# Kernel tuning notes

Measured on AMD Instinct MI355X. Metric: run time of the kernel, lower is better.

Reference implementation:

```python
import jax, jax.numpy as jnp
import numpy as np

N = 100000
E = 1600000
IN_C, HID_C, OUT_C = 64, 64, 32


def setup_inputs() -> dict:
    key = jax.random.key(0)
    ks = jax.random.split(key, 8)
    x = jax.random.normal(ks[0], (N, IN_C), dtype=jnp.float32)
    edge_index = jax.random.randint(ks[1], (2, E), 0, N, dtype=jnp.int64)
    # GCNConv weights (glorot-ish scale) and biases
    W1 = jax.random.normal(ks[2], (IN_C, HID_C), dtype=jnp.float32) / np.sqrt(IN_C)
    b1 = jnp.zeros((HID_C,), dtype=jnp.float32)
    W2 = jax.random.normal(ks[3], (HID_C, HID_C), dtype=jnp.float32) / np.sqrt(HID_C)
    b2 = jnp.zeros((HID_C,), dtype=jnp.float32)
    Wlin = jax.random.normal(ks[4], (HID_C, OUT_C), dtype=jnp.float32) / np.sqrt(HID_C)
    blin = jnp.zeros((OUT_C,), dtype=jnp.float32)
    return {"x": x, "edge_index": edge_index, "W1": W1, "b1": b1,
            "W2": W2, "b2": b2, "Wlin": Wlin, "blin": blin}


def _gcn_norm(edge_index):
    # PyG GCNConv default: add self-loops, symmetric normalization.
    loop = jnp.arange(N, dtype=edge_index.dtype)
    row = jnp.concatenate([edge_index[0], loop])  # source nodes [E+N]
    col = jnp.concatenate([edge_index[1], loop])  # target nodes [E+N]
    deg = jax.ops.segment_sum(jnp.ones_like(col, dtype=jnp.float32), col,
                              num_segments=N)
    dinv = jnp.where(deg > 0, deg ** -0.5, 0.0)
    norm = dinv[row] * dinv[col]  # [E+N]
    return row, col, norm


def _gcn_conv(h, W, b, row, col, norm):
    h = h @ W                                  # [N, F_out]
    msg = h[row] * norm[:, None]               # gather + scale, [E+N, F_out]
    out = jax.ops.segment_sum(msg, col, num_segments=N)  # scatter-add
    return out + b


def reference(x, edge_index, W1, b1, W2, b2, Wlin, blin):
    row, col, norm = _gcn_norm(edge_index)
    h = jax.nn.relu(_gcn_conv(x, W1, b1, row, col, norm))
    h = jax.nn.relu(_gcn_conv(h, W2, b2, row, col, norm))
    return h @ Wlin + blin
```

## Files before the change

kernel.cpp:

```cpp
#include <hip/hip_runtime.h>
#include <hip/hip_fp16.h>

#define IN_C 64
#define HID_C 64
#define OUT_C 32
#define S_NODES  512
#define S_CAP  12288
#define CHUNK_E 4096

typedef _Float16 f16_t;
typedef f16_t f16x2 __attribute__((ext_vector_type(2)));

__device__ __forceinline__ float dot2(unsigned int a, unsigned int b, float c) {
#if __has_builtin(__builtin_amdgcn_fdot2)
    return __builtin_amdgcn_fdot2(*(f16x2*)&a, *(f16x2*)&b, c, false);
#else
    float2 af = __half22float2(*(__half2*)&a);
    float2 bf = __half22float2(*(__half2*)&b);
    return fmaf(af.x, bf.x, fmaf(af.y, bf.y, c));
#endif
}

__device__ __forceinline__ void mix2(float& s0, float& s1, unsigned int p, float w) {
    asm("v_fma_mix_f32 %0, %2, %3, %0 op_sel:[0,0,0] op_sel_hi:[1,0,0]\n\t"
        "v_fma_mix_f32 %1, %2, %3, %1 op_sel:[1,0,0] op_sel_hi:[1,0,0]"
        : "+v"(s0), "+v"(s1)
        : "v"(p), "v"(w));
}

__device__ __forceinline__ int wave_iscan(int x, int lane) {
#pragma unroll
    for (int o = 1; o < 64; o <<= 1) {
        int y = __shfl_up(x, o);
        if (lane >= o) x += y;
    }
    return x;
}

__global__ __launch_bounds__(256) void fat(const void* ei, int E,
                                           int* bcur, int NB,
                                           int* __restrict__ staging,
                                           int NEB, int GB,
                                           const float* __restrict__ x,
                                           const float* __restrict__ W1,
                                           float* __restrict__ t32, int n,
                                           const float* __restrict__ W2,
                                           const float* __restrict__ Wlin,
                                           unsigned short* __restrict__ Wh2,
                                           unsigned short* __restrict__ Whl) {
    __shared__ __align__(16) int smem[5128];
    int tid = threadIdx.x;
    int b = blockIdx.x;
    if (b < NEB) {
        int* cnt = smem;          int* boff = smem + 256;
        int* lcur = smem + 512;   int* gbase = smem + 768;
        int* stg = smem + 1024;
        int* ps64 = smem + 5120;
        int* wsum = smem + 5121;
        int lane = tid & 63, wv = tid >> 6;
        if (tid == 0) *ps64 = 1;
        cnt[tid] = 0;
        __syncthreads();
        if (2 * tid + 1 < 2 * E && ((const int*)ei)[2 * tid + 1] != 0) *ps64 = 0;
        __syncthreads();
        int is64 = *ps64;
        int e0 = b * CHUNK_E;
        int e1 = min(E, e0 + CHUNK_E);
        const int* ei32 = (const int*)ei;
        int rbuf[16];
        int bbuf[16];
        if (is64) {
#pragma unroll
            for (int k = 0; k < 16; k++) {
                int e = e0 + (k << 8) + tid;
                if (e < e1) {
                    int src = ei32[2 * e];
                    int dst = ei32[2 * (E + e)];
                    rbuf[k] = src | ((dst & 511) << 17);
                    int bk = dst >> 9;
                    bbuf[k] = bk;
                    atomicAdd(&cnt[bk], 1);
                } else bbuf[k] = -1;
            }
        } else {
#pragma unroll
            for (int k = 0; k < 16; k++) {
                int e = e0 + (k << 8) + tid;
                if (e < e1) {
                    int src = ei32[e];
                    int dst = ei32[E + e];
                    rbuf[k] = src | ((dst & 511) << 17);
                    int bk = dst >> 9;
                    bbuf[k] = bk;
                    atomicAdd(&cnt[bk], 1);
                } else bbuf[k] = -1;
            }
        }
        __syncthreads();
        int v = cnt[tid];
        int xx = wave_iscan(v, lane);
        if (lane == 63) wsum[wv] = xx;
        __syncthreads();
        int add = 0;
#pragma unroll
        for (int w = 0; w < 3; w++) add += (w < wv) ? wsum[w] : 0;
        int bo = xx + add - v;
        boff[tid] = bo;
        lcur[tid] = bo;
        __syncthreads();
#pragma unroll
        for (int k = 0; k < 16; k++) {
            if (bbuf[k] >= 0) {
                int p = atomicAdd(&lcur[bbuf[k]], 1);
                stg[p] = rbuf[k];
            }
        }
        __syncthreads();
        if (tid < NB && cnt[tid] > 0) gbase[tid] = atomicAdd(&bcur[tid], cnt[tid]);
        __syncthreads();
        int sw = tid >> 4, sl = tid & 15;
        for (int bk = sw; bk < NB; bk += 16) {
            int c = cnt[bk];
            if (c == 0) continue;
            int o = boff[bk], g = gbase[bk];
            size_t gb = (size_t)bk * S_CAP;
            for (int j = sl; j < c; j += 16) {
                if (g + j < S_CAP) staging[gb + g + j] = stg[o + j];
            }
        }
    } else if (b < NEB + GB) {
        uint4* sA = (uint4*)smem;
        int bb = b - NEB;
        int lane = tid & 63, wave = tid >> 6;
        unsigned int wu[32];
#pragma unroll
        for (int k = 0; k < 32; k++) {
            f16x2 p;
            p.x = (f16_t)W1[(2 * k) * 64 + lane];
            p.y = (f16_t)W1[(2 * k + 1) * 64 + lane];
            wu[k] = *(unsigned int*)&p;
        }
        int base = bb * 64;
        const float2* A2 = (const float2*)x;
        int lim = n * 32;
        for (int i = tid; i < 2048; i += 256) {
            int gi = base * 32 + i;
            float2 v = (gi < lim) ? A2[gi] : make_float2(0.f, 0.f);
            ((__half2*)sA)[i] = __floats2half2_rn(v.x, v.y);
        }
        __syncthreads();
        int r0 = base + wave * 16;
        int r1 = min(r0 + 16, n);
        for (int r = r0; r < r1; r++) {
            int rr = r - base;
            float a0 = 0.f, a1 = 0.f;
#pragma unroll
            for (int j = 0; j < 8; j++) {
                uint4 u = sA[rr * 8 + j];
                a0 = dot2(u.x, wu[4 * j], a0);
                a1 = dot2(u.y, wu[4 * j + 1], a1);
                a0 = dot2(u.z, wu[4 * j + 2], a0);
                a1 = dot2(u.w, wu[4 * j + 3], a1);
            }
            t32[(size_t)r * 64 + lane] = a0 + a1;
        }
    } else {
        for (int i = tid; i < 4096; i += 256) {
            int r = i >> 6, c = i & 63;
            f16_t h2 = (f16_t)W2[r * 64 + c];
            Wh2[c * 64 + r] = *(unsigned short*)&h2;
        }
        for (int i = tid; i < 2048; i += 256) {
            int r = i >> 5, c = i & 31;
            f16_t h = (f16_t)Wlin[r * 32 + c];
            Whl[c * 64 + r] = *(unsigned short*)&h;
        }
    }
}

__global__ __launch_bounds__(1024) void place_fine(const int* __restrict__ staging,
                                                   const int* __restrict__ bcur,
                                                   int* __restrict__ offs,
                                                   float* __restrict__ dinv,
                                                   int* __restrict__ rec,
                                                   const float* __restrict__ t32,
                                                   unsigned short* __restrict__ t16,
                                                   int N, int NB) {
    __shared__ int sdeg[S_NODES];
    __shared__ int curs[S_NODES];
    __shared__ int sb[256];
    __shared__ float sdinv[S_NODES];
    __shared__ int wsum[16];
    int tid = threadIdx.x;
    int lane = tid & 63, wv = tid >> 6;
    if (tid < S_NODES) sdeg[tid] = 0;
    if (tid < 256) {
        int v = (tid < NB) ? min(bcur[tid], S_CAP) : 0;
        int xx = wave_iscan(v, lane);
        if (lane == 63) wsum[wv] = xx;
        sb[tid] = xx;
    }
    __syncthreads();
    if (tid < 256) {
        int add = 0;
#pragma unroll
        for (int w = 0; w < 3; w++) add += (w < wv) ? wsum[w] : 0;
        sb[tid] += add;
    }
    __syncthreads();
    int cnt = min(bcur[blockIdx.x], S_CAP);
    int bbase = sb[blockIdx.x] - cnt;
    if (blockIdx.x == NB - 1 && tid == 0) offs[N] = sb[255];
    int base = blockIdx.x * S_NODES;
    int nn = min(S_NODES, N - base);
    size_t sbase = (size_t)blockIdx.x * S_CAP;
    for (int j = tid; j < cnt; j += 1024) atomicAdd(&sdeg[staging[sbase + j] >> 17], 1);
    __syncthreads();
    int d = (tid < S_NODES) ? sdeg[tid] : 0;
    int x2 = wave_iscan(d, lane);
    if (tid < S_NODES && lane == 63) wsum[wv] = x2;
    __syncthreads();
    if (tid < S_NODES) {
        int add2 = 0;
#pragma unroll
        for (int w = 0; w < 7; w++) add2 += (w < wv) ? wsum[w] : 0;
        int pre = bbase + x2 + add2 - d;
        curs[tid] = pre;
        float dv = rsqrtf((float)(d + 1));
        sdinv[tid] = dv;
        if (tid < nn) {
            offs[base + tid] = pre;
            dinv[base + tid] = dv;
        }
    }
    __syncthreads();
    for (int j = tid; j < cnt; j += 1024) {
        int pk = staging[sbase + j];
        int p = atomicAdd(&curs[pk >> 17], 1);
        rec[p] = pk & 0x1FFFF;
    }
    const float4* tin = (const float4*)t32 + (size_t)base * 16;
    uint2* tout = (uint2*)t16 + (size_t)base * 16;
    int jmax = nn * 16;
    for (int j = tid; j < jmax; j += 1024) {
        float4 vv = tin[j];
        float w = sdinv[j >> 4];
        __half2 h0 = __floats2half2_rn(vv.x * w, vv.y * w);
        __half2 h1 = __floats2half2_rn(vv.z * w, vv.w * w);
        tout[j] = make_uint2(*(unsigned int*)&h0, *(unsigned int*)&h1);
    }
}

__device__ __forceinline__ void agg_consume(const uint4& v, float w, float s[8]) {
    mix2(s[0], s[1], v.x, w);
    mix2(s[2], s[3], v.y, w);
    mix2(s[4], s[5], v.z, w);
    mix2(s[6], s[7], v.w, w);
}

template <int NU, bool MASK>
__device__ __forceinline__ void agg_chunk(const uint4* __restrict__ t4,
                                          const int* __restrict__ rec,
                                          int beg, int node, int me, int i,
                                          int g, int gl, float s[8]) {
    int srcs[NU];
    float ws[NU];
    uint4 vs[NU];
#pragma unroll
    for (int u = 0; u < NU; u++) {
        int it = i + u * 8 + g;
        if (MASK) {
            srcs[u] = (it < me) ? rec[beg + it] : node;
            ws[u] = (it < me) ? 1.f : 0.f;
        } else {
            srcs[u] = rec[beg + it];
        }
    }
#pragma unroll
    for (int u = 0; u < NU; u++) vs[u] = t4[(size_t)srcs[u] * 8 + gl];
#pragma unroll
    for (int u = 0; u < NU; u++) agg_consume(vs[u], MASK ? ws[u] : 1.f, s);
}

__global__ void aggregate(const unsigned short* __restrict__ t,
                          const int* __restrict__ offs, const int* __restrict__ rec,
                          const float* __restrict__ dinv, const float* __restrict__ bias,
                          unsigned short* __restrict__ acc, int n) {
    int wave = (blockIdx.x * blockDim.x + threadIdx.x) >> 6;
    int lane = threadIdx.x & 63;
    if (wave >= n) return;
    int g = lane >> 3;
    int gl = lane & 7;
    int beg = offs[wave], end = offs[wave + 1];
    int me = end - beg;
    const uint4* t4 = (const uint4*)t;
    uint4 selfv;
    if (g == 0) selfv = t4[(size_t)wave * 8 + gl];
    float s[8] = {0.f, 0.f, 0.f, 0.f, 0.f, 0.f, 0.f, 0.f};
    int i = 0;
    for (; me - i >= 32; i += 32) agg_chunk<4, false>(t4, rec, beg, wave, me, i, g, gl, s);
    int rem = me - i;
    if (rem > 24)      agg_chunk<4, true>(t4, rec, beg, wave, me, i, g, gl, s);
    else if (rem > 16) agg_chunk<3, true>(t4, rec, beg, wave, me, i, g, gl, s);
    else if (rem > 8)  agg_chunk<2, true>(t4, rec, beg, wave, me, i, g, gl, s);
    else if (rem > 0)  agg_chunk<1, true>(t4, rec, beg, wave, me, i, g, gl, s);
#pragma unroll
    for (int k = 0; k < 8; k++) {
        s[k] += __shfl_xor(s[k], 8);
        s[k] += __shfl_xor(s[k], 16);
        s[k] += __shfl_xor(s[k], 32);
    }
    if (g == 0) {
        agg_consume(selfv, 1.f, s);
        float d = dinv[wave];
        const float4* b4 = (const float4*)bias;
        float4 bb0 = b4[gl * 2], bb1 = b4[gl * 2 + 1];
        float o0 = fmaxf(fmaf(s[0], d, bb0.x), 0.f);
        float o1 = fmaxf(fmaf(s[1], d, bb0.y), 0.f);
        float o2 = fmaxf(fmaf(s[2], d, bb0.z), 0.f);
        float o3 = fmaxf(fmaf(s[3], d, bb0.w), 0.f);
        float o4 = fmaxf(fmaf(s[4], d, bb1.x), 0.f);
        float o5 = fmaxf(fmaf(s[5], d, bb1.y), 0.f);
        float o6 = fmaxf(fmaf(s[6], d, bb1.z), 0.f);
        float o7 = fmaxf(fmaf(s[7], d, bb1.w), 0.f);
        __half2 p0 = __floats2half2_rn(o0, o1);
        __half2 p1 = __floats2half2_rn(o2, o3);
        __half2 p2 = __floats2half2_rn(o4, o5);
        __half2 p3 = __floats2half2_rn(o6, o7);
        ((uint4*)acc)[(size_t)wave * 8 + gl] =
            make_uint4(*(unsigned int*)&p0, *(unsigned int*)&p1,
                       *(unsigned int*)&p2, *(unsigned int*)&p3);
    }
}

__global__ __launch_bounds__(256) void gemm64(const unsigned short* __restrict__ in,
                                              const unsigned short* __restrict__ Wh,
                                              unsigned short* __restrict__ out,
                                              const float* __restrict__ dinv, int n) {
    __shared__ uint4 sA[64 * 8];
    int tid = threadIdx.x;
    int lane = tid & 63, wave = tid >> 6;
    unsigned int wu[32];
    {
        const uint4* col = (const uint4*)(Wh + (size_t)lane * 64);
#pragma unroll
        for (int j = 0; j < 8; j++) {
            uint4 w4 = col[j];
            wu[4 * j] = w4.x; wu[4 * j + 1] = w4.y;
            wu[4 * j + 2] = w4.z; wu[4 * j + 3] = w4.w;
        }
    }
    int base = blockIdx.x * 64;
    const uint2* A2 = (const uint2*)in;
    int lim = n * 16;
    for (int i = tid; i < 1024; i += 256) {
        int gi = base * 16 + i;
        ((uint2*)sA)[i] = (gi < lim) ? A2[gi] : make_uint2(0u, 0u);
    }
    __syncthreads();
    int r0 = base + wave * 16;
    int r1 = min(r0 + 16, n);
    for (int r = r0; r < r1; r++) {
        int rr = r - base;
        float a0 = 0.f, a1 = 0.f;
#pragma unroll
        for (int j = 0; j < 8; j++) {
            uint4 u = sA[rr * 8 + j];
            a0 = dot2(u.x, wu[4 * j], a0);
            a1 = dot2(u.y, wu[4 * j + 1], a1);
            a0 = dot2(u.z, wu[4 * j + 2], a0);
            a1 = dot2(u.w, wu[4 * j + 3], a1);
        }
        __half hv = __float2half_rn((a0 + a1) * dinv[r]);
        out[(size_t)r * 64 + lane] = *(unsigned short*)&hv;
    }
}

__global__ __launch_bounds__(256) void gemm32(const unsigned short* __restrict__ in,
                                              const unsigned short* __restrict__ Wh,
                                              const float* __restrict__ b,
                                              float* __restrict__ out, int n) {
    __shared__ uint4 sA[64 * 8];
    int tid = threadIdx.x;
    int lane = tid & 63, wave = tid >> 6;
    int c = lane & 31;
    unsigned int wu[32];
    {
        const uint4* col = (const uint4*)(Wh + (size_t)c * 64);
#pragma unroll
        for (int j = 0; j < 8; j++) {
            uint4 w4 = col[j];
            wu[4 * j] = w4.x; wu[4 * j + 1] = w4.y;
            wu[4 * j + 2] = w4.z; wu[4 * j + 3] = w4.w;
        }
    }
    float bl = b[c];
    int base = blockIdx.x * 64;
    const uint2* A2 = (const uint2*)in;
    int lim = n * 16;
    for (int i = tid; i < 1024; i += 256) {
        int gi = base * 16 + i;
        ((uint2*)sA)[i] = (gi < lim) ? A2[gi] : make_uint2(0u, 0u);
    }
    __syncthreads();
    int r0 = base + wave * 16;
    int r1 = min(r0 + 16, n);
    for (int r = r0; r < r1; r++) {
        int rr = r - base;
        float a0 = 0.f, a1 = 0.f;
#pragma unroll
        for (int j = 0; j < 8; j++) {
            uint4 u = sA[rr * 8 + j];
            a0 = dot2(u.x, wu[4 * j], a0);
            a1 = dot2(u.y, wu[4 * j + 1], a1);
            a0 = dot2(u.z, wu[4 * j + 2], a0);
            a1 = dot2(u.w, wu[4 * j + 3], a1);
        }
        if (lane < 32) out[(size_t)r * 32 + c] = bl + a0 + a1;
    }
}

extern "C" void kernel_launch(void* const* d_in, const int* in_sizes, int n_in,
                              void* d_out, int out_size, void* d_ws, size_t ws_size,
                              hipStream_t stream) {
    (void)n_in; (void)out_size; (void)ws_size;
    const float* x    = (const float*)d_in[0];
    const void*  ei   = d_in[1];
    const float* W1   = (const float*)d_in[2];
    const float* b1   = (const float*)d_in[3];
    const float* W2   = (const float*)d_in[4];
    const float* b2   = (const float*)d_in[5];
    const float* Wlin = (const float*)d_in[6];
    const float* blin = (const float*)d_in[7];
    float* out = (float*)d_out;

    const int N = in_sizes[0] / IN_C;
    const int E = in_sizes[1] / 2;
    const int NB = (N + S_NODES - 1) / S_NODES;
    const int NEB = (E + CHUNK_E - 1) / CHUNK_E;
    const int GB = (N + 63) / 64;

    char* ws = (char*)d_ws;
    size_t off = 0;
    auto alloc = [&](size_t bytes) -> void* {
        size_t a = (off + 255) & ~(size_t)255;
        off = a + bytes;
        return (void*)(ws + a);
    };
    int*   offs    = (int*)  alloc((size_t)(N + 1) * 4);
    float* dinv    = (float*)alloc((size_t)N * 4);
    int*   bcur    = (int*)  alloc((size_t)NB * 4);
    int*   rec     = (int*)  alloc((size_t)E * 4);
    int*   staging = (int*)  alloc((size_t)NB * S_CAP * 4);
    float* t32     = (float*)alloc((size_t)N * HID_C * 4);
    unsigned short* t16 = (unsigned short*)alloc((size_t)N * HID_C * 2);
    unsigned short* Wh2 = (unsigned short*)alloc(64 * 64 * 2);
    unsigned short* Whl = (unsigned short*)alloc(64 * 32 * 2);
    unsigned short* acc = (unsigned short*)t32;

    hipMemsetAsync(bcur, 0, (size_t)NB * 4, stream);

    fat<<<NEB + GB + 1, 256, 0, stream>>>(ei, E, bcur, NB, staging, NEB, GB,
                                          x, W1, t32, N, W2, Wlin, Wh2, Whl);
    place_fine<<<NB, 1024, 0, stream>>>(staging, bcur, offs, dinv, rec,
                                        t32, t16, N, NB);

    aggregate<<<(N + 3) / 4, 256, 0, stream>>>(t16, offs, rec, dinv, b1, acc, N);
    gemm64<<<GB, 256, 0, stream>>>(acc, Wh2, t16, dinv, N);
    aggregate<<<(N + 3) / 4, 256, 0, stream>>>(t16, offs, rec, dinv, b2, acc, N);
    gemm32<<<GB, 256, 0, stream>>>(acc, Whl, blin, out, N);
}
```

Baseline: 249.6 us.

## Fuse all stages into one persistent cooperative kernel with grid syncs

Replaces the six separate kernel launches with a single cooperative persistent kernel that loops over work items per stage and uses grid.sync between the binning/GEMM1, placement, aggregation and GEMM stages. The goal is to remove launch gaps and tail effects between the short dependent kernels. The placement stage is also reworked from 1024-thread blocks to 256 threads, with two nodes per thread, so that it fits the shared persistent block shape. The trade-off is that occupancy is capped by the largest shared-memory user, and grid-wide barriers cost time. A fallback path with separate kernels is kept for devices that cannot do cooperative launch.

```diff
diff --git a/kernel.cpp b/kernel.cpp
--- a/kernel.cpp
+++ b/kernel.cpp
@@ -1,5 +1,8 @@
 #include <hip/hip_runtime.h>
+#include <hip/hip_cooperative_groups.h>
 #include <hip/hip_fp16.h>
+
+namespace cg = cooperative_groups;
 
 #define IN_C 64
 #define HID_C 64
@@ -37,204 +40,208 @@
     return x;
 }
 
-__global__ __launch_bounds__(256) void fat(const void* ei, int E,
-                                           int* bcur, int NB,
-                                           int* __restrict__ staging,
-                                           int NEB, int GB,
-                                           const float* __restrict__ x,
-                                           const float* __restrict__ W1,
-                                           float* __restrict__ t32, int n,
-                                           const float* __restrict__ W2,
-                                           const float* __restrict__ Wlin,
-                                           unsigned short* __restrict__ Wh2,
-                                           unsigned short* __restrict__ Whl) {
-    __shared__ __align__(16) int smem[5128];
-    int tid = threadIdx.x;
-    int b = blockIdx.x;
-    if (b < NEB) {
-        int* cnt = smem;          int* boff = smem + 256;
-        int* lcur = smem + 512;   int* gbase = smem + 768;
-        int* stg = smem + 1024;
-        int* ps64 = smem + 5120;
-        int* wsum = smem + 5121;
-        int lane = tid & 63, wv = tid >> 6;
-        if (tid == 0) *ps64 = 1;
-        cnt[tid] = 0;
-        __syncthreads();
-        if (2 * tid + 1 < 2 * E && ((const int*)ei)[2 * tid + 1] != 0) *ps64 = 0;
-        __syncthreads();
-        int is64 = *ps64;
-        int e0 = b * CHUNK_E;
-        int e1 = min(E, e0 + CHUNK_E);
-        const int* ei32 = (const int*)ei;
-        int rbuf[16];
-        int bbuf[16];
-        if (is64) {
-#pragma unroll
-            for (int k = 0; k < 16; k++) {
-                int e = e0 + (k << 8) + tid;
-                if (e < e1) {
-                    int src = ei32[2 * e];
-                    int dst = ei32[2 * (E + e)];
-                    rbuf[k] = src | ((dst & 511) << 17);
-                    int bk = dst >> 9;
-                    bbuf[k] = bk;
-                    atomicAdd(&cnt[bk], 1);
-                } else bbuf[k] = -1;
-            }
-        } else {
-#pragma unroll
-            for (int k = 0; k < 16; k++) {
-                int e = e0 + (k << 8) + tid;
-                if (e < e1) {
-                    int src = ei32[e];
-                    int dst = ei32[E + e];
-                    rbuf[k] = src | ((dst & 511) << 17);
-                    int bk = dst >> 9;
-                    bbuf[k] = bk;
-                    atomicAdd(&cnt[bk], 1);
-                } else bbuf[k] = -1;
-            }
-        }
-        __syncthreads();
-        int v = cnt[tid];
-        int xx = wave_iscan(v, lane);
-        if (lane == 63) wsum[wv] = xx;
-        __syncthreads();
-        int add = 0;
-#pragma unroll
-        for (int w = 0; w < 3; w++) add += (w < wv) ? wsum[w] : 0;
-        int bo = xx + add - v;
-        boff[tid] = bo;
-        lcur[tid] = bo;
-        __syncthreads();
-#pragma unroll
-        for (int k = 0; k < 16; k++) {
-            if (bbuf[k] >= 0) {
-                int p = atomicAdd(&lcur[bbuf[k]], 1);
-                stg[p] = rbuf[k];
-            }
-        }
-        __syncthreads();
-        if (tid < NB && cnt[tid] > 0) gbase[tid] = atomicAdd(&bcur[tid], cnt[tid]);
-        __syncthreads();
-        int sw = tid >> 4, sl = tid & 15;
-        for (int bk = sw; bk < NB; bk += 16) {
-            int c = cnt[bk];
-            if (c == 0) continue;
-            int o = boff[bk], g = gbase[bk];
-            size_t gb = (size_t)bk * S_CAP;
-            for (int j = sl; j < c; j += 16) {
-                if (g + j < S_CAP) staging[gb + g + j] = stg[o + j];
-            }
-        }
-    } else if (b < NEB + GB) {
-        uint4* sA = (uint4*)smem;
-        int bb = b - NEB;
-        int lane = tid & 63, wave = tid >> 6;
-        unsigned int wu[32];
-#pragma unroll
-        for (int k = 0; k < 32; k++) {
-            f16x2 p;
-            p.x = (f16_t)W1[(2 * k) * 64 + lane];
-            p.y = (f16_t)W1[(2 * k + 1) * 64 + lane];
-            wu[k] = *(unsigned int*)&p;
-        }
-        int base = bb * 64;
-        const float2* A2 = (const float2*)x;
-        int lim = n * 32;
-        for (int i = tid; i < 2048; i += 256) {
-            int gi = base * 32 + i;
-            float2 v = (gi < lim) ? A2[gi] : make_float2(0.f, 0.f);
-            ((__half2*)sA)[i] = __floats2half2_rn(v.x, v.y);
-        }
-        __syncthreads();
-        int r0 = base + wave * 16;
-        int r1 = min(r0 + 16, n);
-        for (int r = r0; r < r1; r++) {
-            int rr = r - base;
-            float a0 = 0.f, a1 = 0.f;
-#pragma unroll
-            for (int j = 0; j < 8; j++) {
-                uint4 u = sA[rr * 8 + j];
-                a0 = dot2(u.x, wu[4 * j], a0);
-                a1 = dot2(u.y, wu[4 * j + 1], a1);
-                a0 = dot2(u.z, wu[4 * j + 2], a0);
-                a1 = dot2(u.w, wu[4 * j + 3], a1);
-            }
-            t32[(size_t)r * 64 + lane] = a0 + a1;
-        }
-    } else {
-        for (int i = tid; i < 4096; i += 256) {
-            int r = i >> 6, c = i & 63;
-            f16_t h2 = (f16_t)W2[r * 64 + c];
-            Wh2[c * 64 + r] = *(unsigned short*)&h2;
-        }
-        for (int i = tid; i < 2048; i += 256) {
-            int r = i >> 5, c = i & 31;
-            f16_t h = (f16_t)Wlin[r * 32 + c];
-            Whl[c * 64 + r] = *(unsigned short*)&h;
-        }
-    }
-}
-
-__global__ __launch_bounds__(1024) void place_fine(const int* __restrict__ staging,
-                                                   const int* __restrict__ bcur,
-                                                   int* __restrict__ offs,
-                                                   float* __restrict__ dinv,
-                                                   int* __restrict__ rec,
-                                                   const float* __restrict__ t32,
-                                                   unsigned short* __restrict__ t16,
-                                                   int N, int NB) {
-    __shared__ int sdeg[S_NODES];
-    __shared__ int curs[S_NODES];
-    __shared__ int sb[256];
-    __shared__ float sdinv[S_NODES];
-    __shared__ int wsum[16];
+
+__device__ __forceinline__ void dev_bin(int b, int* smem, const void* ei, int E,
+                                        int* bcur, int NB, int* __restrict__ staging) {
+    int* cnt = smem;          int* boff = smem + 256;
+    int* lcur = smem + 512;   int* gbase = smem + 768;
+    int* stg = smem + 1024;
+    int* ps64 = smem + 5120;
+    int* wsum = smem + 5121;
     int tid = threadIdx.x;
     int lane = tid & 63, wv = tid >> 6;
-    if (tid < S_NODES) sdeg[tid] = 0;
-    if (tid < 256) {
-        int v = (tid < NB) ? min(bcur[tid], S_CAP) : 0;
-        int xx = wave_iscan(v, lane);
-        if (lane == 63) wsum[wv] = xx;
-        sb[tid] = xx;
-    }
-    __syncthreads();
-    if (tid < 256) {
-        int add = 0;
-#pragma unroll
-        for (int w = 0; w < 3; w++) add += (w < wv) ? wsum[w] : 0;
-        sb[tid] += add;
-    }
-    __syncthreads();
-    int cnt = min(bcur[blockIdx.x], S_CAP);
-    int bbase = sb[blockIdx.x] - cnt;
-    if (blockIdx.x == NB - 1 && tid == 0) offs[N] = sb[255];
-    int base = blockIdx.x * S_NODES;
+    if (tid == 0) *ps64 = 1;
+    cnt[tid] = 0;
+    __syncthreads();
+    if (2 * tid + 1 < 2 * E && ((const int*)ei)[2 * tid + 1] != 0) *ps64 = 0;
+    __syncthreads();
+    int is64 = *ps64;
+    int e0 = b * CHUNK_E;
+    int e1 = min(E, e0 + CHUNK_E);
+    const int* ei32 = (const int*)ei;
+    int rbuf[16];
+    int bbuf[16];
+    if (is64) {
+#pragma unroll
+        for (int k = 0; k < 16; k++) {
+            int e = e0 + (k << 8) + tid;
+            if (e < e1) {
+                int src = ei32[2 * e];
+                int dst = ei32[2 * (E + e)];
+                rbuf[k] = src | ((dst & 511) << 17);
+                int bk = dst >> 9;
+                bbuf[k] = bk;
+                atomicAdd(&cnt[bk], 1);
+            } else bbuf[k] = -1;
+        }
+    } else {
+#pragma unroll
+        for (int k = 0; k < 16; k++) {
+            int e = e0 + (k << 8) + tid;
+            if (e < e1) {
+                int src = ei32[e];
+                int dst = ei32[E + e];
+                rbuf[k] = src | ((dst & 511) << 17);
+                int bk = dst >> 9;
+                bbuf[k] = bk;
+                atomicAdd(&cnt[bk], 1);
+            } else bbuf[k] = -1;
+        }
+    }
+    __syncthreads();
+    int v = cnt[tid];
+    int xx = wave_iscan(v, lane);
+    if (lane == 63) wsum[wv] = xx;
+    __syncthreads();
+    int add = 0;
+#pragma unroll
+    for (int w = 0; w < 3; w++) add += (w < wv) ? wsum[w] : 0;
+    int bo = xx + add - v;
+    boff[tid] = bo;
+    lcur[tid] = bo;
+    __syncthreads();
+#pragma unroll
+    for (int k = 0; k < 16; k++) {
+        if (bbuf[k] >= 0) {
+            int p = atomicAdd(&lcur[bbuf[k]], 1);
+            stg[p] = rbuf[k];
+        }
+    }
+    __syncthreads();
+    if (tid < NB && cnt[tid] > 0) gbase[tid] = atomicAdd(&bcur[tid], cnt[tid]);
+    __syncthreads();
+    int sw = tid >> 4, sl = tid & 15;
+    for (int bk = sw; bk < NB; bk += 16) {
+        int c = cnt[bk];
+        if (c == 0) continue;
+        int o = boff[bk], g = gbase[bk];
+        size_t gb = (size_t)bk * S_CAP;
+        for (int j = sl; j < c; j += 16) {
+            if (g + j < S_CAP) staging[gb + g + j] = stg[o + j];
+        }
+    }
+    __syncthreads();
+}
+
+__device__ __forceinline__ void dev_gemm1(int bb, int* smem,
+                                          const float* __restrict__ x,
+                                          const float* __restrict__ W1,
+                                          float* __restrict__ t32, int n) {
+    uint4* sA = (uint4*)smem;
+    int tid = threadIdx.x;
+    int lane = tid & 63, wave = tid >> 6;
+    unsigned int wu[32];
+#pragma unroll
+    for (int k = 0; k < 32; k++) {
+        f16x2 p;
+        p.x = (f16_t)W1[(2 * k) * 64 + lane];
+        p.y = (f16_t)W1[(2 * k + 1) * 64 + lane];
+        wu[k] = *(unsigned int*)&p;
+    }
+    int base = bb * 64;
+    const float2* A2 = (const float2*)x;
+    int lim = n * 32;
+    for (int i = tid; i < 2048; i += 256) {
+        int gi = base * 32 + i;
+        float2 v = (gi < lim) ? A2[gi] : make_float2(0.f, 0.f);
+        ((__half2*)sA)[i] = __floats2half2_rn(v.x, v.y);
+    }
+    __syncthreads();
+    int r0 = base + wave * 16;
+    int r1 = min(r0 + 16, n);
+    for (int r = r0; r < r1; r++) {
+        int rr = r - base;
+        float a0 = 0.f, a1 = 0.f;
+#pragma unroll
+        for (int j = 0; j < 8; j++) {
+            uint4 u = sA[rr * 8 + j];
+            a0 = dot2(u.x, wu[4 * j], a0);
+            a1 = dot2(u.y, wu[4 * j + 1], a1);
+            a0 = dot2(u.z, wu[4 * j + 2], a0);
+            a1 = dot2(u.w, wu[4 * j + 3], a1);
+        }
+        t32[(size_t)r * 64 + lane] = a0 + a1;
+    }
+    __syncthreads();
+}
+
+__device__ __forceinline__ void dev_wconv(const float* __restrict__ W2,
+                                          const float* __restrict__ Wlin,
+                                          unsigned short* __restrict__ Wh2,
+                                          unsigned short* __restrict__ Whl) {
+    int tid = threadIdx.x;
+    for (int i = tid; i < 4096; i += 256) {
+        int r = i >> 6, c = i & 63;
+        f16_t h2 = (f16_t)W2[r * 64 + c];
+        Wh2[c * 64 + r] = *(unsigned short*)&h2;
+    }
+    for (int i = tid; i < 2048; i += 256) {
+        int r = i >> 5, c = i & 31;
+        f16_t h = (f16_t)Wlin[r * 32 + c];
+        Whl[c * 64 + r] = *(unsigned short*)&h;
+    }
+}
+
+__device__ __forceinline__ void dev_place(int b, int* smem,
+                                          const int* __restrict__ staging,
+                                          const int* __restrict__ bcur,
+                                          int* __restrict__ offs,
+                                          float* __restrict__ dinv,
+                                          int* __restrict__ rec,
+                                          const float* __restrict__ t32,
+                                          unsigned short* __restrict__ t16,
+                                          int N, int NB) {
+    int* sdeg = smem;
+    int* curs = smem + 512;
+    int* sb   = smem + 1024;
+    float* sdinv = (float*)(smem + 1280);
+    int* wsum = smem + 1792;
+    int tid = threadIdx.x;
+    int lane = tid & 63, wv = tid >> 6;
+    int v = (tid < NB) ? min(bcur[tid], S_CAP) : 0;
+    sdeg[tid] = 0;
+    sdeg[tid + 256] = 0;
+    int xx = wave_iscan(v, lane);
+    if (lane == 63) wsum[wv] = xx;
+    __syncthreads();
+    int add = 0;
+#pragma unroll
+    for (int w = 0; w < 3; w++) add += (w < wv) ? wsum[w] : 0;
+    sb[tid] = xx + add;
+    __syncthreads();
+    int cnt = min(bcur[b], S_CAP);
+    int bbase = sb[b] - cnt;
+    if (b == NB - 1 && tid == 0) offs[N] = sb[255];
+    int base = b * S_NODES;
     int nn = min(S_NODES, N - base);
-    size_t sbase = (size_t)blockIdx.x * S_CAP;
-    for (int j = tid; j < cnt; j += 1024) atomicAdd(&sdeg[staging[sbase + j] >> 17], 1);
-    __syncthreads();
-    int d = (tid < S_NODES) ? sdeg[tid] : 0;
-    int x2 = wave_iscan(d, lane);
-    if (tid < S_NODES && lane == 63) wsum[wv] = x2;
-    __syncthreads();
-    if (tid < S_NODES) {
-        int add2 = 0;
-#pragma unroll
-        for (int w = 0; w < 7; w++) add2 += (w < wv) ? wsum[w] : 0;
-        int pre = bbase + x2 + add2 - d;
-        curs[tid] = pre;
-        float dv = rsqrtf((float)(d + 1));
-        sdinv[tid] = dv;
-        if (tid < nn) {
-            offs[base + tid] = pre;
-            dinv[base + tid] = dv;
-        }
-    }
-    __syncthreads();
-    for (int j = tid; j < cnt; j += 1024) {
+    size_t sbase = (size_t)b * S_CAP;
+    for (int j = tid; j < cnt; j += 256) atomicAdd(&sdeg[staging[sbase + j] >> 17], 1);
+    __syncthreads();
+    int d0 = sdeg[2 * tid], d1 = sdeg[2 * tid + 1];
+    int t = d0 + d1;
+    int x2 = wave_iscan(t, lane);
+    if (lane == 63) wsum[wv] = x2;
+    __syncthreads();
+    int add2 = 0;
+#pragma unroll
+    for (int w = 0; w < 3; w++) add2 += (w < wv) ? wsum[w] : 0;
+    int pre = bbase + x2 + add2 - t;
+    curs[2 * tid] = pre;
+    curs[2 * tid + 1] = pre + d0;
+    float dv0 = rsqrtf((float)(d0 + 1));
+    float dv1 = rsqrtf((float)(d1 + 1));
+    sdinv[2 * tid] = dv0;
+    sdinv[2 * tid + 1] = dv1;
+    if (2 * tid < nn) {
+        offs[base + 2 * tid] = pre;
+        dinv[base + 2 * tid] = dv0;
+    }
+    if (2 * tid + 1 < nn) {
+        offs[base + 2 * tid + 1] = pre + d0;
+        dinv[base + 2 * tid + 1] = dv1;
+    }
+    __syncthreads();
+    for (int j = tid; j < cnt; j += 256) {
         int pk = staging[sbase + j];
         int p = atomicAdd(&curs[pk >> 17], 1);
         rec[p] = pk & 0x1FFFF;
@@ -242,13 +249,14 @@
     const float4* tin = (const float4*)t32 + (size_t)base * 16;
     uint2* tout = (uint2*)t16 + (size_t)base * 16;
     int jmax = nn * 16;
-    for (int j = tid; j < jmax; j += 1024) {
+    for (int j = tid; j < jmax; j += 256) {
         float4 vv = tin[j];
         float w = sdinv[j >> 4];
         __half2 h0 = __floats2half2_rn(vv.x * w, vv.y * w);
         __half2 h1 = __floats2half2_rn(vv.z * w, vv.w * w);
         tout[j] = make_uint2(*(unsigned int*)&h0, *(unsigned int*)&h1);
     }
+    __syncthreads();
 }
 
 __device__ __forceinline__ void agg_consume(const uint4& v, float w, float s[8]) {
@@ -282,11 +290,13 @@
     for (int u = 0; u < NU; u++) agg_consume(vs[u], MASK ? ws[u] : 1.f, s);
 }
 
-__global__ void aggregate(const unsigned short* __restrict__ t,
-                          const int* __restrict__ offs, const int* __restrict__ rec,
-                          const float* __restrict__ dinv, const float* __restrict__ bias,
-                          unsigned short* __restrict__ acc, int n) {
-    int wave = (blockIdx.x * blockDim.x + threadIdx.x) >> 6;
+__device__ __forceinline__ void dev_agg(int q, const unsigned short* __restrict__ t,
+                                        const int* __restrict__ offs,
+                                        const int* __restrict__ rec,
+                                        const float* __restrict__ dinv,
+                                        const float* __restrict__ bias,
+                                        unsigned short* __restrict__ acc, int n) {
+    int wave = q * 4 + (threadIdx.x >> 6);
     int lane = threadIdx.x & 63;
     if (wave >= n) return;
     int g = lane >> 3;
@@ -333,11 +343,12 @@
     }
 }
 
-__global__ __launch_bounds__(256) void gemm64(const unsigned short* __restrict__ in,
-                                              const unsigned short* __restrict__ Wh,
-                                              unsigned short* __restrict__ out,
-                                              const float* __restrict__ dinv, int n) {
-    __shared__ uint4 sA[64 * 8];
+__device__ __forceinline__ void dev_gemm64(int bb, int* smem,
+                                           const unsigned short* __restrict__ in,
+                                           const unsigned short* __restrict__ Wh,
+                                           unsigned short* __restrict__ out,
+                                           const float* __restrict__ dinv, int n) {
+    uint4* sA = (uint4*)smem;
     int tid = threadIdx.x;
     int lane = tid & 63, wave = tid >> 6;
     unsigned int wu[32];
@@ -350,7 +361,7 @@
             wu[4 * j + 2] = w4.z; wu[4 * j + 3] = w4.w;
         }
     }
-    int base = blockIdx.x * 64;
+    int base = bb * 64;
     const uint2* A2 = (const uint2*)in;
     int lim = n * 16;
     for (int i = tid; i < 1024; i += 256) {
@@ -374,13 +385,15 @@
         __half hv = __float2half_rn((a0 + a1) * dinv[r]);
         out[(size_t)r * 64 + lane] = *(unsigned short*)&hv;
     }
-}
-
-__global__ __launch_bounds__(256) void gemm32(const unsigned short* __restrict__ in,
-                                              const unsigned short* __restrict__ Wh,
-                                              const float* __restrict__ b,
-                                              float* __restrict__ out, int n) {
-    __shared__ uint4 sA[64 * 8];
+    __syncthreads();
+}
+
+__device__ __forceinline__ void dev_gemm32(int bb, int* smem,
+                                           const unsigned short* __restrict__ in,
+                                           const unsigned short* __restrict__ Wh,
+                                           const float* __restrict__ b,
+                                           float* __restrict__ out, int n) {
+    uint4* sA = (uint4*)smem;
     int tid = threadIdx.x;
     int lane = tid & 63, wave = tid >> 6;
     int c = lane & 31;
@@ -395,7 +408,7 @@
         }
     }
     float bl = b[c];
-    int base = blockIdx.x * 64;
+    int base = bb * 64;
     const uint2* A2 = (const uint2*)in;
     int lim = n * 16;
     for (int i = tid; i < 1024; i += 256) {
@@ -418,6 +431,85 @@
         }
         if (lane < 32) out[(size_t)r * 32 + c] = bl + a0 + a1;
     }
+    __syncthreads();
+}
+
+__global__ __launch_bounds__(256) void pipeline(
+        const void* ei, int E, int* bcur, int NB, int* staging,
+        int NEB, int GB,
+        const float* x, const float* W1, float* t32,
+        const float* W2, const float* Wlin,
+        unsigned short* Wh2, unsigned short* Whl,
+        int* offs, float* dinv, int* rec, unsigned short* t16,
+        const float* b1, const float* b2, const float* blin,
+        float* out, int N) {
+    __shared__ __align__(16) int smem[5128];
+    cg::grid_group grid = cg::this_grid();
+    unsigned short* acc = (unsigned short*)t32;
+    int NW1 = NEB + GB + 1;
+    for (int wi = blockIdx.x; wi < NW1; wi += gridDim.x) {
+        if (wi < NEB)          dev_bin(wi, smem, ei, E, bcur, NB, staging);
+        else if (wi < NEB + GB) dev_gemm1(wi - NEB, smem, x, W1, t32, N);
+        else                    dev_wconv(W2, Wlin, Wh2, Whl);
+    }
+    grid.sync();
+    for (int wi = blockIdx.x; wi < NB; wi += gridDim.x)
+        dev_place(wi, smem, staging, bcur, offs, dinv, rec, t32, t16, N, NB);
+    grid.sync();
+    int NQ = (N + 3) >> 2;
+    for (int wi = blockIdx.x; wi < NQ; wi += gridDim.x)
+        dev_agg(wi, t16, offs, rec, dinv, b1, acc, N);
+    grid.sync();
+    for (int wi = blockIdx.x; wi < GB; wi += gridDim.x)
+        dev_gemm64(wi, smem, acc, Wh2, t16, dinv, N);
+    grid.sync();
+    for (int wi = blockIdx.x; wi < NQ; wi += gridDim.x)
+        dev_agg(wi, t16, offs, rec, dinv, b2, acc, N);
+    grid.sync();
+    for (int wi = blockIdx.x; wi < GB; wi += gridDim.x)
+        dev_gemm32(wi, smem, acc, Whl, blin, out, N);
+}
+
+__global__ __launch_bounds__(256) void k_fat(const void* ei, int E, int* bcur, int NB,
+                                             int* staging, int NEB, int GB,
+                                             const float* x, const float* W1,
+                                             float* t32, int n,
+                                             const float* W2, const float* Wlin,
+                                             unsigned short* Wh2, unsigned short* Whl) {
+    __shared__ __align__(16) int smem[5128];
+    int b = blockIdx.x;
+    if (b < NEB) dev_bin(b, smem, ei, E, bcur, NB, staging);
+    else if (b < NEB + GB) dev_gemm1(b - NEB, smem, x, W1, t32, n);
+    else dev_wconv(W2, Wlin, Wh2, Whl);
+}
+
+__global__ __launch_bounds__(256) void k_place(const int* staging, const int* bcur,
+                                               int* offs, float* dinv, int* rec,
+                                               const float* t32, unsigned short* t16,
+                                               int N, int NB) {
+    __shared__ __align__(16) int smem[2048];
+    dev_place(blockIdx.x, smem, staging, bcur, offs, dinv, rec, t32, t16, N, NB);
+}
+
+__global__ void k_agg(const unsigned short* t, const int* offs, const int* rec,
+                      const float* dinv, const float* bias,
+                      unsigned short* acc, int n) {
+    dev_agg(blockIdx.x, t, offs, rec, dinv, bias, acc, n);
+}
+
+__global__ __launch_bounds__(256) void k_gemm64(const unsigned short* in,
+                                                const unsigned short* Wh,
+                                                unsigned short* out,
+                                                const float* dinv, int n) {
+    __shared__ __align__(16) int smem[2048];
+    dev_gemm64(blockIdx.x, smem, in, Wh, out, dinv, n);
+}
+
+__global__ __launch_bounds__(256) void k_gemm32(const unsigned short* in,
+                                                const unsigned short* Wh,
+                                                const float* b, float* out, int n) {
+    __shared__ __align__(16) int smem[2048];
+    dev_gemm32(blockIdx.x, smem, in, Wh, b, out, n);
 }
 
 extern "C" void kernel_launch(void* const* d_in, const int* in_sizes, int n_in,
@@ -460,13 +552,44 @@
 
     hipMemsetAsync(bcur, 0, (size_t)NB * 4, stream);
 
-    fat<<<NEB + GB + 1, 256, 0, stream>>>(ei, E, bcur, NB, staging, NEB, GB,
-                                          x, W1, t32, N, W2, Wlin, Wh2, Whl);
-    place_fine<<<NB, 1024, 0, stream>>>(staging, bcur, offs, dinv, rec,
-                                        t32, t16, N, NB);
-
-    aggregate<<<(N + 3) / 4, 256, 0, stream>>>(t16, offs, rec, dinv, b1, acc, N);
-    gemm64<<<GB, 256, 0, stream>>>(acc, Wh2, t16, dinv, N);
-    aggregate<<<(N + 3) / 4, 256, 0, stream>>>(t16, offs, rec, dinv, b2, acc, N);
-    gemm32<<<GB, 256, 0, stream>>>(acc, Whl, blin, out, N);
-}
+    static int g_coop = -1;
+    static int g_grid = 0;
+    if (g_coop < 0) {
+        int dev = 0;
+        hipGetDevice(&dev);
+        int coop = 0;
+        hipDeviceGetAttribute(&coop, hipDeviceAttributeCooperativeLaunch, dev);
+        int maxB = 0, ncu = 0;
+        if (coop) {
+            if (hipOccupancyMaxActiveBlocksPerMultiprocessor(&maxB, pipeline, 256, 0)
+                    != hipSuccess || maxB < 1)
+                coop = 0;
+        }
+        hipDeviceGetAttribute(&ncu, hipDeviceAttributeMultiprocessorCount, dev);
+        if (ncu <= 0) ncu = 256;
+        g_coop = coop;
+        g_grid = maxB * ncu;
+        if (g_grid <= 0) g_coop = 0;
+    }
+
+    if (g_coop) {
+        void* args[] = {
+            (void*)&ei, (void*)&E, (void*)&bcur, (void*)&NB, (void*)&staging,
+            (void*)&NEB, (void*)&GB,
+            (void*)&x, (void*)&W1, (void*)&t32,
+            (void*)&W2, (void*)&Wlin, (void*)&Wh2, (void*)&Whl,
+            (void*)&offs, (void*)&dinv, (void*)&rec, (void*)&t16,
+            (void*)&b1, (void*)&b2, (void*)&blin,
+            (void*)&out, (void*)&N};
+        hipLaunchCooperativeKernel((void*)pipeline, dim3(g_grid), dim3(256),
+                                   args, 0, stream);
+    } else {
+        k_fat<<<NEB + GB + 1, 256, 0, stream>>>(ei, E, bcur, NB, staging, NEB, GB,
+                                                x, W1, t32, N, W2, Wlin, Wh2, Whl);
+        k_place<<<NB, 256, 0, stream>>>(staging, bcur, offs, dinv, rec, t32, t16, N, NB);
+        k_agg<<<(N + 3) / 4, 256, 0, stream>>>(t16, offs, rec, dinv, b1, acc, N);
+        k_gemm64<<<GB, 256, 0, stream>>>(acc, Wh2, t16, dinv, N);
+        k_agg<<<(N + 3) / 4, 256, 0, stream>>>(t16, offs, rec, dinv, b2, acc, N);
+        k_gemm32<<<GB, 256, 0, stream>>>(acc, Whl, blin, out, N);
+    }
+}
```

Result: slower. 776.4 us (+211.1%).
